# Optimization experiments

Hardware: AMD Instinct MI355X
Metric: run time of the kernel (lower is better)

The kernel has to match this reference:

```python
import jax, jax.numpy as jnp
import numpy as np

D, H, DFF, DC = 1024, 16, 4096, 768
DH = D // H
EPS = 1e-5

def layer_norm(x, g, b):
    m = jnp.mean(x, axis=-1, keepdims=True)
    v = jnp.mean(jnp.square(x - m), axis=-1, keepdims=True)
    return (x - m) * jax.lax.rsqrt(v + EPS) * g + b

def setup_inputs() -> dict:
    key = jax.random.key(0)
    ks = jax.random.split(key, 20)
    s = 0.02
    return {
        "x": jax.random.normal(ks[0], (2, 2048, D), jnp.float32),
        "cond": jax.random.normal(ks[1], (2, 77, DC), jnp.float32),
        # self-attention params
        "Wqkv": jax.random.normal(ks[2], (D, 3 * D), jnp.float32) * s,
        "Wproj_sa": jax.random.normal(ks[3], (D, D), jnp.float32) * s,
        "bproj_sa": jnp.zeros((D,), jnp.float32),
        "g1": jnp.ones((D,), jnp.float32),
        "b1": jnp.zeros((D,), jnp.float32),
        # cross-attention params
        "Wq_ca": jax.random.normal(ks[4], (D, D), jnp.float32) * s,
        "Wkv_ca": jax.random.normal(ks[5], (DC, 2 * D), jnp.float32) * s,
        "Wproj_ca": jax.random.normal(ks[6], (D, D), jnp.float32) * s,
        "bproj_ca": jnp.zeros((D,), jnp.float32),
        "g2": jnp.ones((D,), jnp.float32),
        "b2": jnp.zeros((D,), jnp.float32),
        # feed-forward params
        "Wff1": jax.random.normal(ks[7], (D, DFF), jnp.float32) * s,
        "bff1": jnp.zeros((DFF,), jnp.float32),
        "Wff2": jax.random.normal(ks[8], (DFF, D), jnp.float32) * s,
        "bff2": jnp.zeros((D,), jnp.float32),
        "g3": jnp.ones((D,), jnp.float32),
        "b3": jnp.zeros((D,), jnp.float32),
    }

def _self_attn(x, Wqkv, Wproj, bproj):
    B, T, _ = x.shape
    qkv = x @ Wqkv                                   # (B,T,3D)
    qkv = qkv.reshape(B, T, 3, H, DH)
    q, k, v = (qkv[:, :, i].transpose(0, 2, 1, 3) for i in range(3))  # (B,H,T,DH)
    scale = DH ** -0.5
    attn = jnp.einsum('bhtd,bhsd->bhts', q, k) * scale  # (B,H,T,T)
    causal = jnp.triu(jnp.ones((T, T), bool), k=1)
    attn = jnp.where(causal, -jnp.inf, attn)
    attn = jax.nn.softmax(attn, axis=-1)
    out = jnp.einsum('bhts,bhsd->bhtd', attn, v)
    out = out.transpose(0, 2, 1, 3).reshape(B, T, D)
    return out @ Wproj + bproj

def _cross_attn(x, cond, Wq, Wkv, Wproj, bproj):
    B, T, _ = x.shape
    C = cond.shape[1]
    q = (x @ Wq).reshape(B, T, H, DH).transpose(0, 2, 1, 3)      # (B,H,T,DH)
    kv = (cond @ Wkv).reshape(B, C, 2, H, DH)
    k = kv[:, :, 0].transpose(0, 2, 1, 3)                         # (B,H,C,DH)
    v = kv[:, :, 1].transpose(0, 2, 1, 3)
    scale = DH ** -0.5
    attn = jax.nn.softmax(jnp.einsum('bhtd,bhcd->bhtc', q, k) * scale, axis=-1)
    out = jnp.einsum('bhtc,bhcd->bhtd', attn, v)
    out = out.transpose(0, 2, 1, 3).reshape(B, T, D)
    return out @ Wproj + bproj

def reference(x, cond, Wqkv, Wproj_sa, bproj_sa, g1, b1,
              Wq_ca, Wkv_ca, Wproj_ca, bproj_ca, g2, b2,
              Wff1, bff1, Wff2, bff2, g3, b3):
    x = x + _self_attn(layer_norm(x, g1, b1), Wqkv, Wproj_sa, bproj_sa)
    x = x + _cross_attn(layer_norm(x, g2, b2), cond, Wq_ca, Wkv_ca, Wproj_ca, bproj_ca)
    h = layer_norm(x, g3, b3)
    h = jax.nn.gelu(h @ Wff1 + bff1, approximate=False) @ Wff2 + bff2
    return x + h
```

## Files before the change

kernel.cpp:

```cpp
#include <hip/hip_runtime.h>

using bf16   = __bf16;
using bf16x8 = __attribute__((ext_vector_type(8))) bf16;
using f32x4  = __attribute__((ext_vector_type(4))) float;

#define DEV static __device__ __forceinline__

DEV void MFMA16(bf16x8 a, bf16x8 b, f32x4& c){
  c = __builtin_amdgcn_mfma_f32_16x16x32_bf16(a, b, c, 0, 0, 0);
}

DEV void gload16(const bf16* g, bf16* lds){
  __builtin_amdgcn_global_load_lds(
      (const __attribute__((address_space(1))) void*)g,
      (__attribute__((address_space(3))) void*)lds, 16, 0, 0);
}

DEV void tcast_dev(const float* __restrict__ in, bf16* __restrict__ out,
                   int R, int C, int bx, int by, float scale, int nscale,
                   int tid, float (*t)[33])
{
  const int c0 = bx*32, r0 = by*32;
  const int tx = tid & 31, ty = tid >> 5;
  #pragma unroll
  for (int i = ty; i < 32; i += 8) t[i][tx] = in[(size_t)(r0+i)*C + c0+tx];
  __syncthreads();
  #pragma unroll
  for (int i = ty; i < 32; i += 8){
    float v = t[tx][i];
    if (c0 + i < nscale) v *= scale;
    out[(size_t)(c0+i)*R + r0+tx] = (bf16)v;
  }
}

__global__ __launch_bounds__(256) void prep_all(
    const float* Wqkv, bf16* wqkvT, const float* Wps, bf16* wpsT,
    const float* Wqc, bf16* wqcT, const float* Wkvc, bf16* wkvcT,
    const float* Wpc, bf16* wpcT, const float* Wf1, bf16* wf1T,
    const float* Wf2, bf16* wf2T, const float* cond, bf16* condb)
{
  __shared__ float t[32][33];
  const int bid = blockIdx.x, tid = threadIdx.x;
  if (bid < 3072)       tcast_dev(Wqkv, wqkvT, 1024, 3072, bid%96,        bid/96,        0.125f, 1024, tid, t);
  else if (bid < 4096)  tcast_dev(Wps,  wpsT,  1024, 1024, (bid-3072)%32, (bid-3072)/32, 1.f, 0, tid, t);
  else if (bid < 5120)  tcast_dev(Wqc,  wqcT,  1024, 1024, (bid-4096)%32, (bid-4096)/32, 0.125f, 1024, tid, t);
  else if (bid < 6656)  tcast_dev(Wkvc, wkvcT,  768, 2048, (bid-5120)%64, (bid-5120)/64, 1.f, 0, tid, t);
  else if (bid < 7680)  tcast_dev(Wpc,  wpcT,  1024, 1024, (bid-6656)%32, (bid-6656)/32, 1.f, 0, tid, t);
  else if (bid < 11776) tcast_dev(Wf1,  wf1T,  1024, 4096, (bid-7680)%128,(bid-7680)/128,1.f, 0, tid, t);
  else if (bid < 15872) tcast_dev(Wf2,  wf2T,  4096, 1024, (bid-11776)%32,(bid-11776)/32,1.f, 0, tid, t);
  else {
    int i = (bid-15872)*256 + tid;
    condb[i] = (bf16)cond[i];
  }
}

__global__ __launch_bounds__(256) void ln_kernel(const float* __restrict__ x,
    const float* __restrict__ gw, const float* __restrict__ bw, bf16* __restrict__ y)
{
  const int row = blockIdx.x;
  const float4 v = ((const float4*)(x + (size_t)row*1024))[threadIdx.x];
  float s  = v.x+v.y+v.z+v.w;
  float s2 = v.x*v.x+v.y*v.y+v.z*v.z+v.w*v.w;
  #pragma unroll
  for (int off=32; off>=1; off>>=1){ s += __shfl_down(s,off); s2 += __shfl_down(s2,off); }
  __shared__ float red[2][4];
  const int wid = threadIdx.x>>6, lane = threadIdx.x&63;
  if (lane==0){ red[0][wid]=s; red[1][wid]=s2; }
  __syncthreads();
  s  = red[0][0]+red[0][1]+red[0][2]+red[0][3];
  s2 = red[1][0]+red[1][1]+red[1][2]+red[1][3];
  const float m  = s*(1.f/1024.f);
  const float rs = rsqrtf(s2*(1.f/1024.f) - m*m + 1e-5f);
  const float4 gv = ((const float4*)gw)[threadIdx.x];
  const float4 bv = ((const float4*)bw)[threadIdx.x];
  bf16* yr = y + (size_t)row*1024 + threadIdx.x*4;
  yr[0] = (bf16)((v.x-m)*rs*gv.x + bv.x);
  yr[1] = (bf16)((v.y-m)*rs*gv.y + bv.y);
  yr[2] = (bf16)((v.z-m)*rs*gv.z + bv.z);
  yr[3] = (bf16)((v.w-m)*rs*gv.w + bv.w);
}

template<int MODE>
__global__ __launch_bounds__(512) void gemm256(
    const bf16* __restrict__ A, const bf16* __restrict__ Bt,
    const float* __restrict__ bias, const float* resid,
    void* outp, int M, int N, int K)
{
  __shared__ __align__(16) bf16 As[2][256*64];
  __shared__ __align__(16) bf16 Bs[2][256*64];
  const int tid = threadIdx.x;
  const int lane = tid & 63, wid = tid >> 6;
  const int l15 = lane & 15, lh = lane >> 4;
  const int wm = wid >> 2, wn = wid & 3;

  const int nwg = gridDim.x * gridDim.y;
  const int lin = blockIdx.y * gridDim.x + blockIdx.x;
  const int wg  = (lin & 7) * (nwg >> 3) + (lin >> 3);
  const size_t m0 = (size_t)(wg / gridDim.x) * 256;
  const size_t n0 = (size_t)(wg % gridDim.x) * 256;

  f32x4 acc[8][4];
  #pragma unroll
  for (int i=0;i<8;++i)
    #pragma unroll
    for (int j=0;j<4;++j) acc[i][j] = (f32x4){0.f,0.f,0.f,0.f};

  const int srow8 = lane >> 3;
  const int scol  = ((lane & 7) ^ srow8) * 8;

  const int NT = K >> 6;

  #pragma unroll
  for (int i = 0; i < 4; ++i) {
    int r = wid*32 + i*8;
    gload16(A  + (m0 + (size_t)(r + srow8))*K + scol, &As[0][r*64]);
    gload16(Bt + (n0 + (size_t)(r + srow8))*K + scol, &Bs[0][r*64]);
  }
  __syncthreads();

  for (int t = 0; t < NT; ++t) {
    const int cur = t & 1;
    if (t + 1 < NT) {
      const int k0 = (t+1) << 6;
      #pragma unroll
      for (int i = 0; i < 4; ++i) {
        int r = wid*32 + i*8;
        gload16(A  + (m0 + (size_t)(r + srow8))*K + k0 + scol, &As[cur^1][r*64]);
        gload16(Bt + (n0 + (size_t)(r + srow8))*K + k0 + scol, &Bs[cur^1][r*64]);
      }
    }
    #pragma unroll
    for (int kk = 0; kk < 2; ++kk) {
      bf16x8 af[8], bfr[4];
      #pragma unroll
      for (int i=0;i<8;++i){
        const int arow = wm*128 + i*16 + l15;
        af[i]  = *(const bf16x8*)&As[cur][arow*64 + (((kk*4+lh) ^ (arow&7))<<3)];
      }
      #pragma unroll
      for (int n=0;n<4;++n){
        const int brow = wn*64 + n*16 + l15;
        bfr[n] = *(const bf16x8*)&Bs[cur][brow*64 + (((kk*4+lh) ^ (brow&7))<<3)];
      }
      #pragma unroll
      for (int mi=0;mi<8;++mi)
        #pragma unroll
        for (int ni=0;ni<4;++ni)
          MFMA16(af[mi], bfr[ni], acc[mi][ni]);
    }
    __syncthreads();
  }

  #pragma unroll
  for (int mi=0;mi<8;++mi){
    #pragma unroll
    for (int r=0;r<4;++r){
      size_t row = m0 + wm*128 + mi*16 + 4*lh + r;
      #pragma unroll
      for (int ni=0;ni<4;++ni){
        size_t col = n0 + wn*64 + ni*16 + l15;
        float v = acc[mi][ni][r];
        if (MODE==0) ((bf16*)outp)[row*(size_t)N + col] = (bf16)v;
        else if (MODE==1) ((float*)outp)[row*(size_t)N + col] = v + bias[col] + resid[row*(size_t)N + col];
        else { v += bias[col];
               ((bf16*)outp)[row*(size_t)N + col] =
                   (bf16)(0.5f*v*(1.0f + erff(v*0.70710678f))); }
      }
    }
  }
}

template<int MODE>
__global__ __launch_bounds__(256) void gemm_bt(
    const bf16* __restrict__ A, const bf16* __restrict__ Bt,
    const float* __restrict__ bias, const float* resid,
    void* outp, int M, int N, int K)
{
  __shared__ __align__(16) bf16 As[2][128*64];
  __shared__ __align__(16) bf16 Bs[2][128*64];
  const int tid = threadIdx.x;
  const int lane = tid & 63, wid = tid >> 6;
  const int l15 = lane & 15, lh = lane >> 4;
  const int wm = wid >> 1, wn = wid & 1;

  const int nwg = gridDim.x * gridDim.y;
  const int lin = blockIdx.y * gridDim.x + blockIdx.x;
  const int wg  = (lin & 7) * (nwg >> 3) + (lin >> 3);
  const size_t m0 = (size_t)(wg / gridDim.x) * 128;
  const size_t n0 = (size_t)(wg % gridDim.x) * 128;

  f32x4 acc[4][4];
  #pragma unroll
  for (int i=0;i<4;++i)
    #pragma unroll
    for (int j=0;j<4;++j) acc[i][j] = (f32x4){0.f,0.f,0.f,0.f};

  const int srow8 = lane >> 3;
  const int scol  = ((lane & 7) ^ srow8) * 8;

  const int NT = K >> 6;

  #pragma unroll
  for (int i = 0; i < 4; ++i) {
    int r = wid*32 + i*8;
    int ar = (int)m0 + r + srow8; if (ar >= M) ar = M - 1;
    gload16(A  + (size_t)ar*K + scol,                 &As[0][r*64]);
    gload16(Bt + (n0 + (size_t)(r + srow8))*K + scol, &Bs[0][r*64]);
  }
  __syncthreads();

  for (int t = 0; t < NT; ++t) {
    const int cur = t & 1;
    if (t + 1 < NT) {
      const int k0 = (t+1) << 6;
      #pragma unroll
      for (int i = 0; i < 4; ++i) {
        int r = wid*32 + i*8;
        int ar = (int)m0 + r + srow8; if (ar >= M) ar = M - 1;
        gload16(A  + (size_t)ar*K + k0 + scol,                 &As[cur^1][r*64]);
        gload16(Bt + (n0 + (size_t)(r + srow8))*K + k0 + scol, &Bs[cur^1][r*64]);
      }
    }
    #pragma unroll
    for (int kk = 0; kk < 2; ++kk) {
      bf16x8 af[4], bfr[4];
      #pragma unroll
      for (int i=0;i<4;++i){
        const int arow = wm*64 + i*16 + l15;
        const int brow = wn*64 + i*16 + l15;
        af[i]  = *(const bf16x8*)&As[cur][arow*64 + (((kk*4+lh) ^ (arow&7))<<3)];
        bfr[i] = *(const bf16x8*)&Bs[cur][brow*64 + (((kk*4+lh) ^ (brow&7))<<3)];
      }
      #pragma unroll
      for (int mi=0;mi<4;++mi)
        #pragma unroll
        for (int ni=0;ni<4;++ni)
          MFMA16(af[mi], bfr[ni], acc[mi][ni]);
    }
    __syncthreads();
  }

  #pragma unroll
  for (int mi=0;mi<4;++mi){
    #pragma unroll
    for (int r=0;r<4;++r){
      size_t row = m0 + wm*64 + mi*16 + 4*lh + r;
      if (row < (size_t)M) {
        #pragma unroll
        for (int ni=0;ni<4;++ni){
          size_t col = n0 + wn*64 + ni*16 + l15;
          float v = acc[mi][ni][r];
          if (MODE==0) ((bf16*)outp)[row*(size_t)N + col] = (bf16)v;
          else if (MODE==1) ((float*)outp)[row*(size_t)N + col] = v + bias[col] + resid[row*(size_t)N + col];
          else { v += bias[col];
                 ((bf16*)outp)[row*(size_t)N + col] =
                     (bf16)(0.5f*v*(1.0f + erff(v*0.70710678f))); }
        }
      }
    }
  }
}

template<int MODE>
__global__ __launch_bounds__(256) void gemm32(
    const bf16* __restrict__ A, const bf16* __restrict__ Bt,
    const float* __restrict__ bias, const float* resid,
    void* outp, int M, int N, int K)
{
  __shared__ __align__(16) bf16 As[2][32*64];
  __shared__ __align__(16) bf16 Bs[2][128*64];
  const int tid = threadIdx.x;
  const int lane = tid & 63, wid = tid >> 6;
  const int l15 = lane & 15, lh = lane >> 4;

  const int nwg = gridDim.x * gridDim.y;
  const int lin = blockIdx.y * gridDim.x + blockIdx.x;
  const int wg  = (lin & 7) * (nwg >> 3) + (lin >> 3);
  const size_t m0 = (size_t)(wg / gridDim.x) * 32;
  const size_t n0 = (size_t)(wg % gridDim.x) * 128;

  f32x4 acc[2][2];
  #pragma unroll
  for (int i=0;i<2;++i)
    #pragma unroll
    for (int j=0;j<2;++j) acc[i][j] = (f32x4){0.f,0.f,0.f,0.f};

  const int srow8 = lane >> 3;
  const int scol  = ((lane & 7) ^ srow8) * 8;

  const int NT = K >> 6;

  #pragma unroll
  for (int i = 0; i < 1; ++i) {
    int r = wid*8;
    gload16(A + (m0 + (size_t)(r + srow8))*K + scol, &As[0][r*64]);
  }
  #pragma unroll
  for (int i = 0; i < 4; ++i) {
    int r = wid*32 + i*8;
    gload16(Bt + (n0 + (size_t)(r + srow8))*K + scol, &Bs[0][r*64]);
  }
  __syncthreads();

  for (int t = 0; t < NT; ++t) {
    const int cur = t & 1;
    if (t + 1 < NT) {
      const int k0 = (t+1) << 6;
      {
        int r = wid*8;
        gload16(A + (m0 + (size_t)(r + srow8))*K + k0 + scol, &As[cur^1][r*64]);
      }
      #pragma unroll
      for (int i = 0; i < 4; ++i) {
        int r = wid*32 + i*8;
        gload16(Bt + (n0 + (size_t)(r + srow8))*K + k0 + scol, &Bs[cur^1][r*64]);
      }
    }
    #pragma unroll
    for (int kk = 0; kk < 2; ++kk) {
      bf16x8 af[2], bfr[2];
      #pragma unroll
      for (int i=0;i<2;++i){
        const int arow = i*16 + l15;
        af[i]  = *(const bf16x8*)&As[cur][arow*64 + (((kk*4+lh) ^ (arow&7))<<3)];
      }
      #pragma unroll
      for (int n=0;n<2;++n){
        const int brow = wid*32 + n*16 + l15;
        bfr[n] = *(const bf16x8*)&Bs[cur][brow*64 + (((kk*4+lh) ^ (brow&7))<<3)];
      }
      #pragma unroll
      for (int mi=0;mi<2;++mi)
        #pragma unroll
        for (int ni=0;ni<2;++ni)
          MFMA16(af[mi], bfr[ni], acc[mi][ni]);
    }
    __syncthreads();
  }

  #pragma unroll
  for (int mi=0;mi<2;++mi){
    #pragma unroll
    for (int r=0;r<4;++r){
      size_t row = m0 + mi*16 + 4*lh + r;
      #pragma unroll
      for (int ni=0;ni<2;++ni){
        size_t col = n0 + wid*32 + ni*16 + l15;
        float v = acc[mi][ni][r];
        if (MODE==0) ((bf16*)outp)[row*(size_t)N + col] = (bf16)v;
        else if (MODE==1) ((float*)outp)[row*(size_t)N + col] = v + bias[col] + resid[row*(size_t)N + col];
        else { v += bias[col];
               ((bf16*)outp)[row*(size_t)N + col] =
                   (bf16)(0.5f*v*(1.0f + erff(v*0.70710678f))); }
      }
    }
  }
}

__global__ __launch_bounds__(256) void vtsa_kernel(const bf16* __restrict__ qkv, bf16* __restrict__ vt)
{
  __shared__ bf16 t[32][33];
  const int b = blockIdx.z >> 4, h = blockIdx.z & 15;
  const int s0 = blockIdx.x*32, d0 = blockIdx.y*32;
  const int tx = threadIdx.x & 31, ty = threadIdx.x >> 5;
  #pragma unroll
  for (int i = ty; i < 32; i += 8)
    t[i][tx] = qkv[(size_t)(b*2048 + s0+i)*3072 + 2048 + h*64 + d0 + tx];
  __syncthreads();
  #pragma unroll
  for (int i = ty; i < 32; i += 8)
    vt[((size_t)blockIdx.z*64 + d0+i)*2048 + s0 + tx] = t[tx][i];
}

__global__ __launch_bounds__(256) void kvca_re(const bf16* __restrict__ kvca,
    bf16* __restrict__ kpad, bf16* __restrict__ vtca)
{
  int idx = blockIdx.x*256 + threadIdx.x;
  if (idx >= 2*16*128*64) return;
  int d = idx & 63, s = (idx>>6) & 127, h = (idx>>13) & 15, b = idx>>17;
  bf16 kv = (bf16)0.f, vv = (bf16)0.f;
  if (s < 77) {
    kv = kvca[(size_t)(b*77+s)*2048 + h*64 + d];
    vv = kvca[(size_t)(b*77+s)*2048 + 1024 + h*64 + d];
  }
  kpad[idx] = kv;
  vtca[(((size_t)(b*16+h)*64 + d)<<7) + s] = vv;
}

template<int CAUSAL>
__global__ __launch_bounds__(256) void flash6(
    const bf16* __restrict__ qb, long q_bstride, long qstride,
    const bf16* __restrict__ kb0, long k_bstride, long k_hstride, long kstride,
    const bf16* __restrict__ vtb, long vt_bhstride, long vtstride,
    bf16* __restrict__ out, int skv)
{
  __shared__ __align__(16) bf16 Ks[2][64*64];
  __shared__ __align__(16) bf16 Vs[2][64*64];
  __shared__ __align__(16) bf16 Ps[4][16*68];
  const int tid = threadIdx.x;
  const int w = tid >> 6, lane = tid & 63, l15 = lane & 15, lh = lane >> 4;
  const int bid = blockIdx.x;
  const int bh   = (bid & 7) + 8*((bid >> 3) & 3);
  const int tile = 31 - (bid >> 5);
  const int b = bh >> 4, h = bh & 15;
  const int q0 = tile * 64;
  const int nkb   = CAUSAL ? tile + 1 : ((skv + 63) >> 6);
  const int nfull = CAUSAL ? tile     : (skv >> 6);

  const bf16* kbase = kb0 + (size_t)b*k_bstride + (size_t)h*k_hstride;
  const bf16* vbase = vtb + (size_t)bh*vt_bhstride;
  const int sr0 = tid >> 3, sslot = tid & 7;

  const bf16* qrow = qb + (size_t)b*q_bstride + (size_t)h*64
                        + (size_t)(q0 + w*16 + l15)*qstride;
  bf16x8 qf0 = *(const bf16x8*)(qrow + 8*lh);
  bf16x8 qf1 = *(const bf16x8*)(qrow + 32 + 8*lh);

  f32x4 o[4];
  #pragma unroll
  for (int i=0;i<4;++i) o[i] = (f32x4){0.f,0.f,0.f,0.f};
  float lacc[4] = {0.f,0.f,0.f,0.f};

  bf16x8 kreg[2], vreg[2];
  #pragma unroll
  for (int i=0;i<2;++i){
    int r = sr0 + 32*i;
    kreg[i] = *(const bf16x8*)(kbase + (size_t)r*kstride + sslot*8);
    vreg[i] = *(const bf16x8*)(vbase + (size_t)r*vtstride + sslot*8);
  }

  for (int kb = 0; kb < nkb; ++kb) {
    const int buf = kb & 1;
    #pragma unroll
    for (int i=0;i<2;++i){
      int r = sr0 + 32*i;
      int ps = (sslot ^ (r & 7)) * 8;
      *(bf16x8*)&Ks[buf][r*64 + ps] = kreg[i];
      *(bf16x8*)&Vs[buf][r*64 + ps] = vreg[i];
    }
    __syncthreads();
    if (kb + 1 < nkb) {
      #pragma unroll
      for (int i=0;i<2;++i){
        int r = sr0 + 32*i;
        kreg[i] = *(const bf16x8*)(kbase + (size_t)((kb+1)*64 + r)*kstride + sslot*8);
        vreg[i] = *(const bf16x8*)(vbase + (size_t)r*vtstride + (kb+1)*64 + sslot*8);
      }
    }
    f32x4 sf[4];
    __builtin_amdgcn_s_setprio(1);
    #pragma unroll
    for (int ni = 0; ni < 4; ++ni) {
      int kr = ni*16 + l15;
      bf16x8 kf0 = *(const bf16x8*)&Ks[buf][kr*64 + (((lh  ) ^ (kr&7))<<3)];
      bf16x8 kf1 = *(const bf16x8*)&Ks[buf][kr*64 + (((lh+4) ^ (kr&7))<<3)];
      f32x4 z = (f32x4){0.f,0.f,0.f,0.f};
      MFMA16(qf0, kf0, z);
      MFMA16(qf1, kf1, z);
      sf[ni] = z;
    }
    __builtin_amdgcn_s_setprio(0);
    if (kb >= nfull) {
      #pragma unroll
      for (int ni=0;ni<4;++ni){
        int col = kb*64 + ni*16 + l15;
        #pragma unroll
        for (int r=0;r<4;++r){
          int rowg = q0 + w*16 + 4*lh + r;
          if (col >= skv || (CAUSAL && col > rowg)) sf[ni][r] = -1e30f;
        }
      }
    }
    #pragma unroll
    for (int ni=0;ni<4;++ni){
      #pragma unroll
      for (int r=0;r<4;++r){
        float p = __expf(sf[ni][r]);
        lacc[r] += p;
        Ps[w][(4*lh + r)*68 + ni*16 + l15] = (bf16)p;
      }
    }
    bf16x8 pa0 = *(const bf16x8*)&Ps[w][l15*68 + 8*lh];
    bf16x8 pa1 = *(const bf16x8*)&Ps[w][l15*68 + 32 + 8*lh];
    __builtin_amdgcn_s_setprio(1);
    #pragma unroll
    for (int nd=0;nd<4;++nd){
      int vr = nd*16 + l15;
      bf16x8 vf0 = *(const bf16x8*)&Vs[buf][vr*64 + (((lh  ) ^ (vr&7))<<3)];
      bf16x8 vf1 = *(const bf16x8*)&Vs[buf][vr*64 + (((lh+4) ^ (vr&7))<<3)];
      MFMA16(pa0, vf0, o[nd]);
      MFMA16(pa1, vf1, o[nd]);
    }
    __builtin_amdgcn_s_setprio(0);
  }
  float lr[4];
  #pragma unroll
  for (int r=0;r<4;++r) lr[r] = lacc[r];
  #pragma unroll
  for (int off=1; off<16; off<<=1)
    #pragma unroll
    for (int r=0;r<4;++r) lr[r] += __shfl_xor(lr[r], off);
  #pragma unroll
  for (int nd=0;nd<4;++nd)
    #pragma unroll
    for (int r=0;r<4;++r){
      int rowg = q0 + w*16 + 4*lh + r;
      out[(size_t)(b*2048 + rowg)*1024 + h*64 + nd*16 + l15] =
          (bf16)(o[nd][r] / lr[r]);
    }
}

struct Bump { char* base; size_t off;
  void* get(size_t bytes){ void* p = base + off; off += (bytes + 255) & ~(size_t)255; return p; } };

extern "C" void kernel_launch(void* const* d_in, const int* in_sizes, int n_in,
                              void* d_out, int out_size, void* d_ws, size_t ws_size,
                              hipStream_t stream)
{
  const float* x        = (const float*)d_in[0];
  const float* cond     = (const float*)d_in[1];
  const float* Wqkv     = (const float*)d_in[2];
  const float* Wproj_sa = (const float*)d_in[3];
  const float* bproj_sa = (const float*)d_in[4];
  const float* g1       = (const float*)d_in[5];
  const float* b1       = (const float*)d_in[6];
  const float* Wq_ca    = (const float*)d_in[7];
  const float* Wkv_ca   = (const float*)d_in[8];
  const float* Wproj_ca = (const float*)d_in[9];
  const float* bproj_ca = (const float*)d_in[10];
  const float* g2       = (const float*)d_in[11];
  const float* b2       = (const float*)d_in[12];
  const float* Wff1     = (const float*)d_in[13];
  const float* bff1     = (const float*)d_in[14];
  const float* Wff2     = (const float*)d_in[15];
  const float* bff2     = (const float*)d_in[16];
  const float* g3       = (const float*)d_in[17];
  const float* b3       = (const float*)d_in[18];

  Bump bump{(char*)d_ws, 0};
  bf16* wqkvT    = (bf16*)bump.get((size_t)3072*1024*2);
  bf16* wprojSaT = (bf16*)bump.get((size_t)1024*1024*2);
  bf16* wqCaT    = (bf16*)bump.get((size_t)1024*1024*2);
  bf16* wkvCaT   = (bf16*)bump.get((size_t)2048*768*2);
  bf16* wprojCaT = (bf16*)bump.get((size_t)1024*1024*2);
  bf16* wff1T    = (bf16*)bump.get((size_t)4096*1024*2);
  bf16* wff2T    = (bf16*)bump.get((size_t)1024*4096*2);
  bf16* condb    = (bf16*)bump.get((size_t)154*768*2);
  bf16* xn       = (bf16*)bump.get((size_t)4096*1024*2);
  bf16* qkv      = (bf16*)bump.get((size_t)4096*3072*2);
  bf16* vt_sa    = (bf16*)bump.get((size_t)2*16*64*2048*2);
  bf16* attn     = (bf16*)bump.get((size_t)4096*1024*2);
  bf16* kvca     = (bf16*)bump.get((size_t)154*2048*2);
  bf16* kpad     = (bf16*)bump.get((size_t)2*16*128*64*2);
  bf16* vtca     = (bf16*)bump.get((size_t)2*16*64*128*2);
  bf16* h1   = qkv;
  bf16* qca  = vt_sa;
  float* x1  = (float*)d_out;

  prep_all<<<dim3(16334), 256, 0, stream>>>(
      Wqkv, wqkvT, Wproj_sa, wprojSaT, Wq_ca, wqCaT, Wkv_ca, wkvCaT,
      Wproj_ca, wprojCaT, Wff1, wff1T, Wff2, wff2T, cond, condb);

  ln_kernel<<<dim3(4096), 256, 0, stream>>>(x, g1, b1, xn);
  gemm256<0><<<dim3(12,16), 512, 0, stream>>>(xn, wqkvT, nullptr, nullptr, qkv, 4096, 3072, 1024);
  vtsa_kernel<<<dim3(64,2,32), 256, 0, stream>>>(qkv, vt_sa);
  flash6<1><<<dim3(1024), 256, 0, stream>>>(
      qkv,        (long)2048*3072, 3072,
      qkv + 1024, (long)2048*3072, 64, 3072,
      vt_sa,      (long)64*2048, 2048,
      attn, 2048);
  gemm32<1><<<dim3(8,128), 256, 0, stream>>>(attn, wprojSaT, bproj_sa, x, x1, 4096, 1024, 1024);

  ln_kernel<<<dim3(4096), 256, 0, stream>>>(x1, g2, b2, xn);
  gemm32<0><<<dim3(8,128), 256, 0, stream>>>(xn, wqCaT, nullptr, nullptr, qca, 4096, 1024, 1024);
  gemm_bt<0><<<dim3(16,2), 256, 0, stream>>>(condb, wkvCaT, nullptr, nullptr, kvca, 154, 2048, 768);
  kvca_re<<<dim3(1024), 256, 0, stream>>>(kvca, kpad, vtca);
  flash6<0><<<dim3(1024), 256, 0, stream>>>(
      qca,  (long)2048*1024, 1024,
      kpad, (long)16*128*64, (long)128*64, 64,
      vtca, (long)64*128, 128,
      attn, 77);
  gemm32<1><<<dim3(8,128), 256, 0, stream>>>(attn, wprojCaT, bproj_ca, x1, x1, 4096, 1024, 1024);

  ln_kernel<<<dim3(4096), 256, 0, stream>>>(x1, g3, b3, xn);
  gemm256<2><<<dim3(16,16), 512, 0, stream>>>(xn, wff1T, bff1, nullptr, h1, 4096, 4096, 1024);
  gemm32<1><<<dim3(8,128), 256, 0, stream>>>(h1, wff2T, bff2, x1, d_out, 4096, 1024, 4096);

  (void)in_sizes; (void)n_in; (void)out_size; (void)ws_size;
}
```

Measured before the change: 314.3 us.

## Software-pipeline gemm256 with split half-tile loads, barriers and priority hints

```diff
diff --git a/kernel.cpp b/kernel.cpp
--- a/kernel.cpp
+++ b/kernel.cpp
@@ -81,7 +81,7 @@
 }
 
 template<int MODE>
-__global__ __launch_bounds__(512) void gemm256(
+__global__ __launch_bounds__(512) void gemm256p(
     const bf16* __restrict__ A, const bf16* __restrict__ Bt,
     const float* __restrict__ bias, const float* resid,
     void* outp, int M, int N, int K)
@@ -107,48 +107,89 @@
 
   const int srow8 = lane >> 3;
   const int scol  = ((lane & 7) ^ srow8) * 8;
-
   const int NT = K >> 6;
 
-  #pragma unroll
-  for (int i = 0; i < 4; ++i) {
-    int r = wid*32 + i*8;
-    gload16(A  + (m0 + (size_t)(r + srow8))*K + scol, &As[0][r*64]);
-    gload16(Bt + (n0 + (size_t)(r + srow8))*K + scol, &Bs[0][r*64]);
-  }
-  __syncthreads();
+  auto stageH = [&](int t, int j){
+    if (t >= NT) return;
+    const int k0 = t << 6;
+    const int buf = t & 1;
+    const int hl = j & 1;
+    const bf16* src = (j < 2) ? A : Bt;
+    const size_t base = (j < 2) ? m0 : n0;
+    bf16* dst = (j < 2) ? &As[buf][0] : &Bs[buf][0];
+    #pragma unroll
+    for (int i = 0; i < 2; ++i) {
+      int r = hl*128 + wid*16 + i*8;
+      gload16(src + (base + (size_t)(r + srow8))*K + k0 + scol, dst + r*64);
+    }
+  };
+  auto rdA = [&](int buf, int mh, int kk, bf16x8* dst){
+    #pragma unroll
+    for (int i=0;i<4;++i){
+      int row = wm*128 + (mh*4+i)*16 + l15;
+      dst[i] = *(const bf16x8*)&As[buf][row*64 + (((kk*4+lh) ^ (row&7))<<3)];
+    }
+  };
+  auto rdB = [&](int buf, int kk, bf16x8* dst){
+    #pragma unroll
+    for (int n=0;n<4;++n){
+      int row = wn*64 + n*16 + l15;
+      dst[n] = *(const bf16x8*)&Bs[buf][row*64 + (((kk*4+lh) ^ (row&7))<<3)];
+    }
+  };
+
+  stageH(0,0); stageH(0,1); stageH(0,2); stageH(0,3);
+  stageH(1,0); stageH(1,1);
+  if (NT > 1) asm volatile("s_waitcnt vmcnt(4)" ::: "memory");
+  else        asm volatile("s_waitcnt vmcnt(0)" ::: "memory");
+  __builtin_amdgcn_sched_barrier(0);
+  __builtin_amdgcn_s_barrier();
 
   for (int t = 0; t < NT; ++t) {
-    const int cur = t & 1;
-    if (t + 1 < NT) {
-      const int k0 = (t+1) << 6;
-      #pragma unroll
-      for (int i = 0; i < 4; ++i) {
-        int r = wid*32 + i*8;
-        gload16(A  + (m0 + (size_t)(r + srow8))*K + k0 + scol, &As[cur^1][r*64]);
-        gload16(Bt + (n0 + (size_t)(r + srow8))*K + k0 + scol, &Bs[cur^1][r*64]);
-      }
-    }
-    #pragma unroll
-    for (int kk = 0; kk < 2; ++kk) {
-      bf16x8 af[8], bfr[4];
-      #pragma unroll
-      for (int i=0;i<8;++i){
-        const int arow = wm*128 + i*16 + l15;
-        af[i]  = *(const bf16x8*)&As[cur][arow*64 + (((kk*4+lh) ^ (arow&7))<<3)];
-      }
-      #pragma unroll
-      for (int n=0;n<4;++n){
-        const int brow = wn*64 + n*16 + l15;
-        bfr[n] = *(const bf16x8*)&Bs[cur][brow*64 + (((kk*4+lh) ^ (brow&7))<<3)];
-      }
-      #pragma unroll
-      for (int mi=0;mi<8;++mi)
-        #pragma unroll
-        for (int ni=0;ni<4;++ni)
-          MFMA16(af[mi], bfr[ni], acc[mi][ni]);
-    }
-    __syncthreads();
+    const int buf = t & 1;
+    bf16x8 af0k0[4], af0k1[4], af1k0[4], af1k1[4], bfr0[4], bfr1[4];
+    rdA(buf,0,0,af0k0); rdA(buf,0,1,af0k1); rdB(buf,0,bfr0);
+    stageH(t+1,2);
+    __builtin_amdgcn_s_barrier();
+    asm volatile("s_waitcnt lgkmcnt(0)" ::: "memory");
+    __builtin_amdgcn_sched_barrier(0);
+    __builtin_amdgcn_s_setprio(1);
+    #pragma unroll
+    for (int mi=0;mi<4;++mi)
+      #pragma unroll
+      for (int ni=0;ni<4;++ni) MFMA16(af0k0[mi], bfr0[ni], acc[mi][ni]);
+    __builtin_amdgcn_s_setprio(0);
+    __builtin_amdgcn_sched_barrier(0);
+    __builtin_amdgcn_s_barrier();
+    rdA(buf,1,0,af1k0); rdA(buf,1,1,af1k1); rdB(buf,1,bfr1);
+    stageH(t+1,3);
+    __builtin_amdgcn_s_barrier();
+    asm volatile("s_waitcnt lgkmcnt(0)" ::: "memory");
+    __builtin_amdgcn_sched_barrier(0);
+    __builtin_amdgcn_s_setprio(1);
+    #pragma unroll
+    for (int mi=0;mi<4;++mi)
+      #pragma unroll
+      for (int ni=0;ni<4;++ni) MFMA16(af1k0[mi], bfr0[ni], acc[4+mi][ni]);
+    __builtin_amdgcn_s_setprio(0);
+    __builtin_amdgcn_sched_barrier(0);
+    __builtin_amdgcn_s_barrier();
+    stageH(t+2,0);
+    stageH(t+2,1);
+    __builtin_amdgcn_s_setprio(1);
+    #pragma unroll
+    for (int mi=0;mi<4;++mi)
+      #pragma unroll
+      for (int ni=0;ni<4;++ni) MFMA16(af0k1[mi], bfr1[ni], acc[mi][ni]);
+    #pragma unroll
+    for (int mi=0;mi<4;++mi)
+      #pragma unroll
+      for (int ni=0;ni<4;++ni) MFMA16(af1k1[mi], bfr1[ni], acc[4+mi][ni]);
+    __builtin_amdgcn_s_setprio(0);
+    if (t + 2 < NT) asm volatile("s_waitcnt vmcnt(4)" ::: "memory");
+    else            asm volatile("s_waitcnt vmcnt(0)" ::: "memory");
+    __builtin_amdgcn_sched_barrier(0);
+    __builtin_amdgcn_s_barrier();
   }
 
   #pragma unroll
@@ -290,8 +331,7 @@
 
   const int NT = K >> 6;
 
-  #pragma unroll
-  for (int i = 0; i < 1; ++i) {
+  {
     int r = wid*8;
     gload16(A + (m0 + (size_t)(r + srow8))*K + scol, &As[0][r*64]);
   }
@@ -562,7 +602,7 @@
       Wproj_ca, wprojCaT, Wff1, wff1T, Wff2, wff2T, cond, condb);
 
   ln_kernel<<<dim3(4096), 256, 0, stream>>>(x, g1, b1, xn);
-  gemm256<0><<<dim3(12,16), 512, 0, stream>>>(xn, wqkvT, nullptr, nullptr, qkv, 4096, 3072, 1024);
+  gemm256p<0><<<dim3(12,16), 512, 0, stream>>>(xn, wqkvT, nullptr, nullptr, qkv, 4096, 3072, 1024);
   vtsa_kernel<<<dim3(64,2,32), 256, 0, stream>>>(qkv, vt_sa);
   flash6<1><<<dim3(1024), 256, 0, stream>>>(
       qkv,        (long)2048*3072, 3072,
@@ -583,7 +623,7 @@
   gemm32<1><<<dim3(8,128), 256, 0, stream>>>(attn, wprojCaT, bproj_ca, x1, x1, 4096, 1024, 1024);
 
   ln_kernel<<<dim3(4096), 256, 0, stream>>>(x1, g3, b3, xn);
-  gemm256<2><<<dim3(16,16), 512, 0, stream>>>(xn, wff1T, bff1, nullptr, h1, 4096, 4096, 1024);
+  gemm256p<2><<<dim3(16,16), 512, 0, stream>>>(xn, wff1T, bff1, nullptr, h1, 4096, 4096, 1024);
   gemm32<1><<<dim3(8,128), 256, 0, stream>>>(h1, wff2T, bff2, x1, d_out, 4096, 1024, 4096);
 
   (void)in_sizes; (void)n_in; (void)out_size; (void)ws_size;
```

Result: no change. 309.1 us (-1.7%).
